# Kernel tuning notes

Measured on AMD Instinct MI355X. Metric: run time of the kernel, lower is better.

Reference implementation:

```python
import jax, jax.numpy as jnp
import numpy as np

S, B, I, H, O = 512, 256, 64, 512, 25

def setup_inputs() -> dict:
    key = jax.random.key(0)
    ks = jax.random.split(key, 7)
    k = 1.0 / np.sqrt(H)  # torch nn.RNN / nn.Linear default init bound
    x = jax.random.normal(ks[0], (S, B, I), dtype=jnp.float32)
    W_ih = jax.random.uniform(ks[1], (H, I), jnp.float32, -k, k)
    W_hh = jax.random.uniform(ks[2], (H, H), jnp.float32, -k, k)
    b_ih = jax.random.uniform(ks[3], (H,), jnp.float32, -k, k)
    b_hh = jax.random.uniform(ks[4], (H,), jnp.float32, -k, k)
    W2 = jax.random.uniform(ks[5], (O, H), jnp.float32, -k, k)
    b2 = jax.random.uniform(ks[6], (O,), jnp.float32, -k, k)
    return {"x": x, "W_ih": W_ih, "W_hh": W_hh, "b_ih": b_ih, "b_hh": b_hh, "W2": W2, "b2": b2}

def reference(x, W_ih, W_hh, b_ih, b_hh, W2, b2):
    # Precompute input projection for all timesteps in one big GEMM: (S,B,H)
    xi = jnp.einsum('sbi,hi->sbh', x, W_ih) + b_ih
    h0 = jnp.zeros((x.shape[1], W_hh.shape[0]), dtype=x.dtype)
    W_hh_T = W_hh.T
    def step(h_prev, xi_t):
        h = jax.nn.relu(xi_t + h_prev @ W_hh_T + b_hh)
        return h, h
    _, out = jax.lax.scan(step, h0, xi)  # out: (S, B, H)
    # Faithful to original: out[:, -1, :] selects last batch element -> (S, H)
    y = out[:, -1, :] @ W2.T + b2  # (S, 25)
    return y
```

## Files before the change

### kernel.cpp

```cpp
#include <hip/hip_runtime.h>


#define S_ 512
#define B_ 256
#define I_ 64
#define H_ 512
#define O_ 25
#define G_ 16
#define R_ 32

__global__ __launch_bounds__(256) void rnn_pre(
    const float* __restrict__ x, const float* __restrict__ W_ih,
    const float* __restrict__ b_ih, const float* __restrict__ b_hh,
    float* __restrict__ xi) {
  const int t = blockIdx.x;
  const int tid = threadIdx.x;
  const int o = blockIdx.y * 256 + tid;
  __shared__ float xr[I_];
  if (tid < I_) xr[tid] = x[(t * B_ + (B_ - 1)) * I_ + tid];
  __syncthreads();
  float acc = b_ih[o] + b_hh[o];
  const float4* wp = (const float4*)(W_ih + o * I_);
#pragma unroll
  for (int j = 0; j < I_ / 4; ++j) {
    float4 w4 = wp[j];
    acc += w4.x * xr[4 * j] + w4.y * xr[4 * j + 1] + w4.z * xr[4 * j + 2] +
           w4.w * xr[4 * j + 3];
  }
  xi[t * H_ + o] = acc;
}

__global__ __launch_bounds__(256) void rnn_seq(
    const float* __restrict__ W_hh, const float* __restrict__ xi,
    float* __restrict__ hseq, unsigned long long* hg64) {
  const int tid = threadIdx.x;
  const int b = blockIdx.x;
  const int r = tid & 31;
  const int seg = tid >> 5;
  const int row = b * R_ + r;
  const int k0 = seg * 64;
  const int wave = tid >> 6;

  __shared__ float h_l[H_];
  __shared__ float part[4 * R_];

  float w[64];
  {
    const float4* wp = (const float4*)(W_hh + row * H_ + k0);
#pragma unroll
    for (int j = 0; j < 16; ++j) {
      float4 v = wp[j];
      w[4 * j] = v.x; w[4 * j + 1] = v.y; w[4 * j + 2] = v.z; w[4 * j + 3] = v.w;
    }
  }
  for (int n = tid; n < H_; n += 256) h_l[n] = 0.0f;
  __syncthreads();

  for (int s = 0; s < S_; ++s) {
    float xiv = 0.0f;
    if (tid < R_) xiv = xi[s * H_ + b * R_ + r];

    float acc = 0.0f;
    const float4* hp = (const float4*)(h_l + k0);
#pragma unroll
    for (int j = 0; j < 16; ++j) {
      float4 hv = hp[j];
      acc = fmaf(w[4 * j], hv.x, acc);
      acc = fmaf(w[4 * j + 1], hv.y, acc);
      acc = fmaf(w[4 * j + 2], hv.z, acc);
      acc = fmaf(w[4 * j + 3], hv.w, acc);
    }
    acc += __shfl_xor(acc, 32, 64);
    if ((tid & 32) == 0) part[wave * R_ + r] = acc;
    __syncthreads();

    const int tag = s + 1;
    unsigned long long* buf = hg64 + (tag & 1) * H_;

    if (tid < R_) {
      float sum = part[r] + part[R_ + r] + part[2 * R_ + r] + part[3 * R_ + r] + xiv;
      float h = fmaxf(sum, 0.0f);
      hseq[s * H_ + b * R_ + r] = h;
      unsigned long long pk = ((unsigned long long)(unsigned)tag << 32) |
                              (unsigned long long)__float_as_uint(h);
      __hip_atomic_store(&buf[b * R_ + r], pk, __ATOMIC_RELAXED,
                         __HIP_MEMORY_SCOPE_AGENT);
    }

    for (int n = tid; n < H_; n += 256) {
      unsigned long long p;
      do {
        p = __hip_atomic_load(&buf[n], __ATOMIC_RELAXED, __HIP_MEMORY_SCOPE_AGENT);
      } while ((int)(unsigned)(p >> 32) != tag);
      h_l[n] = __uint_as_float((unsigned)p);
    }
    __syncthreads();
  }
}

__global__ __launch_bounds__(256) void rnn_post(
    const float* __restrict__ hseq, const float* __restrict__ W2,
    const float* __restrict__ b2, float* __restrict__ y) {
  const int t = blockIdx.x;
  const int tid = threadIdx.x;
  __shared__ float hl[H_];
  __shared__ float part[256];
  for (int n = tid; n < H_; n += 256) hl[n] = hseq[t * H_ + n];
  __syncthreads();
  const int o = tid >> 3;
  const int seg = tid & 7;
  float acc = 0.0f;
  if (o < O_) {
    const float4* wp = (const float4*)(W2 + o * H_ + seg * 64);
    const float4* hp = (const float4*)(hl + seg * 64);
#pragma unroll
    for (int j = 0; j < 16; ++j) {
      float4 w4 = wp[j];
      float4 h4 = hp[j];
      acc += w4.x * h4.x + w4.y * h4.y + w4.z * h4.z + w4.w * h4.w;
    }
  }
  part[tid] = acc;
  __syncthreads();
  if (tid < O_) {
    float sum = 0.0f;
#pragma unroll
    for (int j = 0; j < 8; ++j) sum += part[tid * 8 + j];
    y[t * O_ + tid] = sum + b2[tid];
  }
}

extern "C" void kernel_launch(void* const* d_in, const int* in_sizes, int n_in,
                              void* d_out, int out_size, void* d_ws, size_t ws_size,
                              hipStream_t stream) {
  const float* x    = (const float*)d_in[0];
  const float* W_ih = (const float*)d_in[1];
  const float* W_hh = (const float*)d_in[2];
  const float* b_ih = (const float*)d_in[3];
  const float* b_hh = (const float*)d_in[4];
  const float* W2   = (const float*)d_in[5];
  const float* b2   = (const float*)d_in[6];
  float* y = (float*)d_out;

  float* xi   = (float*)d_ws;
  float* hseq = xi + S_ * H_;
  unsigned long long* hg64 = (unsigned long long*)(hseq + S_ * H_);

  rnn_pre<<<dim3(S_, 2), 256, 0, stream>>>(x, W_ih, b_ih, b_hh, xi);
  rnn_seq<<<G_, 256, 0, stream>>>(W_hh, xi, hseq, hg64);
  rnn_post<<<S_, 256, 0, stream>>>(hseq, W2, b2, y);
}
```

Measured before the change: 911.0 us.

## Pack RNN step flag into hidden-state sign bit and skip polling own rows

Cross-block hidden-state exchange now uses 32-bit words whose sign bit carries a phase flag, instead of 64-bit tag+value pairs. This works because ReLU outputs are non-negative. The flags are initialized in the pre kernel. Each block writes its own rows directly into shared memory and polls only foreign entries, issuing both loads per iteration. The next step's xi load is prefetched before the spin-wait, and the dot product is split into four accumulators to shorten the FMA dependency chain. The sign-bit trick depends on h being non-negative, and -0.0 edge cases could cause issues.

```diff
diff --git a/kernel.cpp b/kernel.cpp
--- a/kernel.cpp
+++ b/kernel.cpp
@@ -12,10 +12,16 @@
 __global__ __launch_bounds__(256) void rnn_pre(
     const float* __restrict__ x, const float* __restrict__ W_ih,
     const float* __restrict__ b_ih, const float* __restrict__ b_hh,
-    float* __restrict__ xi) {
+    float* __restrict__ xi, unsigned* __restrict__ hg) {
   const int t = blockIdx.x;
   const int tid = threadIdx.x;
   const int o = blockIdx.y * 256 + tid;
+  if (t == 0 && blockIdx.y == 0) {
+    hg[tid] = 0x80000000u;
+    hg[tid + 256] = 0x80000000u;
+    hg[tid + 512] = 0x80000000u;
+    hg[tid + 768] = 0x80000000u;
+  }
   __shared__ float xr[I_];
   if (tid < I_) xr[tid] = x[(t * B_ + (B_ - 1)) * I_ + tid];
   __syncthreads();
@@ -32,7 +38,7 @@
 
 __global__ __launch_bounds__(256) void rnn_seq(
     const float* __restrict__ W_hh, const float* __restrict__ xi,
-    float* __restrict__ hseq, unsigned long long* hg64) {
+    float* __restrict__ hseq, unsigned* __restrict__ hg) {
   const int tid = threadIdx.x;
   const int b = blockIdx.x;
   const int r = tid & 31;
@@ -40,6 +46,8 @@
   const int row = b * R_ + r;
   const int k0 = seg * 64;
   const int wave = tid >> 6;
+  const int own_lo = b * R_;
+  const int own_hi = b * R_ + R_;
 
   __shared__ float h_l[H_];
   __shared__ float part[4 * R_];
@@ -54,45 +62,63 @@
     }
   }
   for (int n = tid; n < H_; n += 256) h_l[n] = 0.0f;
+
+  float xiv = (tid < R_) ? xi[own_lo + tid] : 0.0f;
   __syncthreads();
 
+  const int n0 = tid, n1 = tid + 256;
+  const bool own0 = (n0 >= own_lo && n0 < own_hi);
+  const bool own1 = (n1 >= own_lo && n1 < own_hi);
+
   for (int s = 0; s < S_; ++s) {
-    float xiv = 0.0f;
-    if (tid < R_) xiv = xi[s * H_ + b * R_ + r];
-
-    float acc = 0.0f;
+    float a0 = 0.f, a1 = 0.f, a2 = 0.f, a3 = 0.f;
     const float4* hp = (const float4*)(h_l + k0);
 #pragma unroll
     for (int j = 0; j < 16; ++j) {
       float4 hv = hp[j];
-      acc = fmaf(w[4 * j], hv.x, acc);
-      acc = fmaf(w[4 * j + 1], hv.y, acc);
-      acc = fmaf(w[4 * j + 2], hv.z, acc);
-      acc = fmaf(w[4 * j + 3], hv.w, acc);
+      a0 = fmaf(w[4 * j + 0], hv.x, a0);
+      a1 = fmaf(w[4 * j + 1], hv.y, a1);
+      a2 = fmaf(w[4 * j + 2], hv.z, a2);
+      a3 = fmaf(w[4 * j + 3], hv.w, a3);
     }
+    float acc = (a0 + a1) + (a2 + a3);
     acc += __shfl_xor(acc, 32, 64);
     if ((tid & 32) == 0) part[wave * R_ + r] = acc;
     __syncthreads();
 
-    const int tag = s + 1;
-    unsigned long long* buf = hg64 + (tag & 1) * H_;
+    const unsigned phase = (unsigned)((s >> 1) & 1);
+    unsigned* buf = hg + (s & 1) * H_;
 
     if (tid < R_) {
-      float sum = part[r] + part[R_ + r] + part[2 * R_ + r] + part[3 * R_ + r] + xiv;
+      float sum = part[tid] + part[R_ + tid] + part[2 * R_ + tid] +
+                  part[3 * R_ + tid] + xiv;
       float h = fmaxf(sum, 0.0f);
-      hseq[s * H_ + b * R_ + r] = h;
-      unsigned long long pk = ((unsigned long long)(unsigned)tag << 32) |
-                              (unsigned long long)__float_as_uint(h);
-      __hip_atomic_store(&buf[b * R_ + r], pk, __ATOMIC_RELAXED,
-                         __HIP_MEMORY_SCOPE_AGENT);
+      h_l[own_lo + tid] = h;
+      hseq[s * H_ + own_lo + tid] = h;
+      __hip_atomic_store(&buf[own_lo + tid],
+                         __float_as_uint(h) | (phase << 31),
+                         __ATOMIC_RELAXED, __HIP_MEMORY_SCOPE_AGENT);
     }
 
-    for (int n = tid; n < H_; n += 256) {
-      unsigned long long p;
-      do {
-        p = __hip_atomic_load(&buf[n], __ATOMIC_RELAXED, __HIP_MEMORY_SCOPE_AGENT);
-      } while ((int)(unsigned)(p >> 32) != tag);
-      h_l[n] = __uint_as_float((unsigned)p);
+    if (s == S_ - 1) break;
+
+    if (tid < R_) xiv = xi[(s + 1) * H_ + own_lo + tid];
+
+    bool need0 = !own0, need1 = !own1;
+    unsigned p0, p1;
+    while (need0 | need1) {
+      if (need0)
+        p0 = __hip_atomic_load(&buf[n0], __ATOMIC_RELAXED, __HIP_MEMORY_SCOPE_AGENT);
+      if (need1)
+        p1 = __hip_atomic_load(&buf[n1], __ATOMIC_RELAXED, __HIP_MEMORY_SCOPE_AGENT);
+      if (need0 && (p0 >> 31) == phase) {
+        h_l[n0] = __uint_as_float(p0 & 0x7fffffffu);
+        need0 = false;
+      }
+      if (need1 && (p1 >> 31) == phase) {
+        h_l[n1] = __uint_as_float(p1 & 0x7fffffffu);
+        need1 = false;
+      }
     }
     __syncthreads();
   }
@@ -144,9 +170,9 @@
 
   float* xi   = (float*)d_ws;
   float* hseq = xi + S_ * H_;
-  unsigned long long* hg64 = (unsigned long long*)(hseq + S_ * H_);
+  unsigned* hg = (unsigned*)(hseq + S_ * H_);
 
-  rnn_pre<<<dim3(S_, 2), 256, 0, stream>>>(x, W_ih, b_ih, b_hh, xi);
-  rnn_seq<<<G_, 256, 0, stream>>>(W_hh, xi, hseq, hg64);
+  rnn_pre<<<dim3(S_, 2), 256, 0, stream>>>(x, W_ih, b_ih, b_hh, xi, hg);
+  rnn_seq<<<G_, 256, 0, stream>>>(W_hh, xi, hseq, hg);
   rnn_post<<<S_, 256, 0, stream>>>(hseq, W2, b2, y);
 }
```

Result: faster. 819.6 us (-10.0%).
